# Optimization experiments

Hardware: AMD Instinct MI355X
Metric: run time of the kernel (lower is better)

Reference implementation:

```python
import jax, jax.numpy as jnp
import numpy as np


def setup_inputs() -> dict:
    key = jax.random.key(0)
    k_x, k_W, k_b, k_ids, k_w = jax.random.split(key, 5)
    N_ADAPTERS, D_OUT, D_IN = 32, 1024, 1024
    B, S = 2, 2048
    K = 8  # number of active adapters
    x = jax.random.normal(k_x, (B, S, D_IN), dtype=jnp.float32)
    W = jax.random.normal(k_W, (N_ADAPTERS, D_OUT, D_IN), dtype=jnp.float32)
    b = jax.random.normal(k_b, (N_ADAPTERS, D_OUT), dtype=jnp.float32)
    ids = jax.random.randint(k_ids, (K,), 0, N_ADAPTERS, dtype=jnp.int64)
    weights = jax.random.uniform(k_w, (K,), dtype=jnp.float32)
    return {"x": x, "W": W, "b": b, "ids": ids, "weights": weights}


def reference(x, W, b, ids, weights):
    # Original: out_i = Linear_{ids[i]}(x); output = sum_i weights[i] * out_i
    Wsel = W[ids]  # [k, o, d]  gather of selected adapter weights
    bsel = b[ids]  # [k, o]
    # Fused weighted mixture of k small GEMMs (same math as loop + weighted sum)
    out = jnp.einsum("k,kod,bsd->bso", weights, Wsel, x)
    out = out + jnp.einsum("k,ko->o", weights, bsel)
    return out
```

## Files before the change

kernel.cpp:

```cpp
#include <hip/hip_runtime.h>
#include <hip/hip_bf16.h>
#include <stdint.h>


typedef __attribute__((ext_vector_type(8))) short short8;
typedef __attribute__((ext_vector_type(4))) float float4v;

#define DIMK 1024
#define DIMN 1024
#define DIMM 4096

__device__ __forceinline__ unsigned short f2bf_rtn(float f) {
  union { float f; unsigned u; } v; v.f = f;
  unsigned u = v.u;
  return (unsigned short)((u + 0x7fffu + ((u >> 16) & 1u)) >> 16);
}

__global__ __launch_bounds__(256) void prep_kernel(
    const float* __restrict__ x, const float* __restrict__ W,
    const float* __restrict__ bia, const int* __restrict__ ids,
    const float* __restrict__ wts,
    unsigned short* __restrict__ xb, unsigned short* __restrict__ Wc,
    float* __restrict__ bc, int K)
{
  const int bid = blockIdx.x;
  if (bid < 1024) {
    const int t  = bid * 256 + threadIdx.x;
    const int o  = t >> 8;
    const int d4 = (t & 255) << 2;
    float ax = 0.f, ay = 0.f, az = 0.f, aw = 0.f;
    for (int k = 0; k < K; ++k) {
      const float wk = wts[k];
      const float4 w4 = *reinterpret_cast<const float4*>(
          &W[((size_t)ids[k] << 20) + ((size_t)o << 10) + d4]);
      ax += wk * w4.x; ay += wk * w4.y; az += wk * w4.z; aw += wk * w4.w;
    }
    ushort4 r;
    r.x = f2bf_rtn(ax); r.y = f2bf_rtn(ay); r.z = f2bf_rtn(az); r.w = f2bf_rtn(aw);
    *reinterpret_cast<ushort4*>(&Wc[(size_t)t << 2]) = r;
    if (t < DIMN) {
      float s = 0.f;
      for (int k = 0; k < K; ++k) s += wts[k] * bia[ids[k] * DIMN + t];
      bc[t] = s;
    }
  } else {
    const size_t t = (size_t)(bid - 1024) * 256 + threadIdx.x;
    const float4 v = *reinterpret_cast<const float4*>(&x[t << 2]);
    ushort4 r;
    r.x = f2bf_rtn(v.x); r.y = f2bf_rtn(v.y); r.z = f2bf_rtn(v.z); r.w = f2bf_rtn(v.w);
    *reinterpret_cast<ushort4*>(&xb[t << 2]) = r;
  }
}

__device__ __forceinline__ void load_lds16(const void* g, void* l) {
  __builtin_amdgcn_global_load_lds(
      (const __attribute__((address_space(1))) void*)g,
      (__attribute__((address_space(3))) void*)l, 16, 0, 0);
}

__global__ __launch_bounds__(256) void gemm_kernel(
    const unsigned short* __restrict__ xb,
    const unsigned short* __restrict__ Wc,
    const float* __restrict__ bc,
    float* __restrict__ out)
{
  constexpr int BK = 32;
  __shared__ __align__(16) unsigned short As[128 * BK];
  __shared__ __align__(16) unsigned short Bs[128 * BK];

  const int tid  = threadIdx.x;
  const int wave = tid >> 6;
  const int lane = tid & 63;
  const int m0 = blockIdx.y * 128;
  const int n0 = blockIdx.x * 128;

  const int crow = lane >> 2;
  const int ccol = (lane & 3) << 3;
  const int cid0 = wave * 2;
  const unsigned short* gA0 = xb + (size_t)(m0 + cid0 * 16 + crow) * DIMK + ccol;
  const unsigned short* gA1 = gA0 + 16 * DIMK;
  const unsigned short* gB0 = Wc + (size_t)(n0 + cid0 * 16 + crow) * DIMK + ccol;
  const unsigned short* gB1 = gB0 + 16 * DIMK;
  unsigned short* lA0 = &As[cid0 * 512];
  unsigned short* lA1 = &As[cid0 * 512 + 512];
  unsigned short* lB0 = &Bs[cid0 * 512];
  unsigned short* lB1 = &Bs[cid0 * 512 + 512];

  const int wm0  = (wave >> 1) * 64;
  const int wn0  = (wave & 1) * 64;
  const int quad = lane >> 4;
  const int r16  = lane & 15;

  const float4v zero = {0.f, 0.f, 0.f, 0.f};
  float4v acc[4][4];
#pragma unroll
  for (int i = 0; i < 4; ++i)
#pragma unroll
    for (int j = 0; j < 4; ++j) acc[i][j] = zero;

  for (int k0 = 0; k0 < DIMK; k0 += BK) {
    load_lds16(gA0 + k0, lA0);
    load_lds16(gA1 + k0, lA1);
    load_lds16(gB0 + k0, lB0);
    load_lds16(gB1 + k0, lB1);
    __syncthreads();

    short8 af[4], bf[4];
#pragma unroll
    for (int mt = 0; mt < 4; ++mt)
      af[mt] = *reinterpret_cast<const short8*>(&As[(wm0 + mt * 16 + r16) * BK + quad * 8]);
#pragma unroll
    for (int nt = 0; nt < 4; ++nt)
      bf[nt] = *reinterpret_cast<const short8*>(&Bs[(wn0 + nt * 16 + r16) * BK + quad * 8]);

#pragma unroll
    for (int mt = 0; mt < 4; ++mt)
#pragma unroll
      for (int nt = 0; nt < 4; ++nt)
        acc[mt][nt] = __builtin_amdgcn_mfma_f32_16x16x32_bf16(af[mt], bf[nt], acc[mt][nt], 0, 0, 0);

    __syncthreads();
  }

#pragma unroll
  for (int nt = 0; nt < 4; ++nt) {
    const int col = n0 + wn0 + nt * 16 + r16;
    const float bias = bc[col];
#pragma unroll
    for (int mt = 0; mt < 4; ++mt) {
      const int rbase = m0 + wm0 + mt * 16 + quad * 4;
#pragma unroll
      for (int r = 0; r < 4; ++r)
        out[(size_t)(rbase + r) * DIMN + col] = acc[mt][nt][r] + bias;
    }
  }
}

extern "C" void kernel_launch(void* const* d_in, const int* in_sizes, int n_in,
                              void* d_out, int out_size, void* d_ws, size_t ws_size,
                              hipStream_t stream) {
  const float* x   = (const float*)d_in[0];
  const float* W   = (const float*)d_in[1];
  const float* b   = (const float*)d_in[2];
  const int*   ids = (const int*)d_in[3];
  const float* wts = (const float*)d_in[4];
  float* out = (float*)d_out;
  const int K = in_sizes[3];

  unsigned short* xb = (unsigned short*)d_ws;
  unsigned short* Wc = (unsigned short*)((char*)d_ws + (8u << 20));
  float*          bc = (float*)((char*)d_ws + (10u << 20));

  prep_kernel<<<5120, 256, 0, stream>>>(x, W, b, ids, wts, xb, Wc, bc, K);
  dim3 grid(DIMN / 128, DIMM / 128);
  gemm_kernel<<<grid, 256, 0, stream>>>(xb, Wc, bc, out);
}
```

Measured before the change: 209.3 us.

## Shrink GEMM M-tile to 64, double BK to 64, and XOR-swizzle LDS layout

```diff
diff --git a/kernel.cpp b/kernel.cpp
--- a/kernel.cpp
+++ b/kernel.cpp
@@ -58,43 +58,49 @@
       (__attribute__((address_space(3))) void*)l, 16, 0, 0);
 }
 
-__global__ __launch_bounds__(256) void gemm_kernel(
+__global__ __launch_bounds__(256, 2) void gemm_kernel(
     const unsigned short* __restrict__ xb,
     const unsigned short* __restrict__ Wc,
     const float* __restrict__ bc,
     float* __restrict__ out)
 {
-  constexpr int BK = 32;
-  __shared__ __align__(16) unsigned short As[128 * BK];
+  constexpr int BK = 64;
+  __shared__ __align__(16) unsigned short As[64 * BK];
   __shared__ __align__(16) unsigned short Bs[128 * BK];
 
   const int tid  = threadIdx.x;
   const int wave = tid >> 6;
   const int lane = tid & 63;
-  const int m0 = blockIdx.y * 128;
+  const int m0 = blockIdx.y * 64;
   const int n0 = blockIdx.x * 128;
 
-  const int crow = lane >> 2;
-  const int ccol = (lane & 3) << 3;
-  const int cid0 = wave * 2;
-  const unsigned short* gA0 = xb + (size_t)(m0 + cid0 * 16 + crow) * DIMK + ccol;
-  const unsigned short* gA1 = gA0 + 16 * DIMK;
-  const unsigned short* gB0 = Wc + (size_t)(n0 + cid0 * 16 + crow) * DIMK + ccol;
-  const unsigned short* gB1 = gB0 + 16 * DIMK;
-  unsigned short* lA0 = &As[cid0 * 512];
-  unsigned short* lA1 = &As[cid0 * 512 + 512];
-  unsigned short* lB0 = &Bs[cid0 * 512];
-  unsigned short* lB1 = &Bs[cid0 * 512 + 512];
+  const int srow = lane >> 3;
+  const int scol = (((lane & 7) ^ srow) << 3);
+  const unsigned short* gA0 = xb + (size_t)(m0 + wave * 16 + srow) * DIMK + scol;
+  const unsigned short* gA1 = gA0 + 8 * DIMK;
+  const unsigned short* gB0 = Wc + (size_t)(n0 + wave * 32 + srow) * DIMK + scol;
+  const unsigned short* gB1 = gB0 + 8 * DIMK;
+  const unsigned short* gB2 = gB0 + 16 * DIMK;
+  const unsigned short* gB3 = gB0 + 24 * DIMK;
+  unsigned short* lA0 = &As[wave * 16 * BK];
+  unsigned short* lA1 = lA0 + 8 * BK;
+  unsigned short* lB0 = &Bs[wave * 32 * BK];
+  unsigned short* lB1 = lB0 + 8 * BK;
+  unsigned short* lB2 = lB0 + 16 * BK;
+  unsigned short* lB3 = lB0 + 24 * BK;
 
-  const int wm0  = (wave >> 1) * 64;
-  const int wn0  = (wave & 1) * 64;
+  const int wm   = (wave >> 1) * 32;
+  const int wn   = (wave & 1) * 64;
   const int quad = lane >> 4;
   const int r16  = lane & 15;
+  const int rx   = r16 & 7;
+  const int po0  = ((quad ^ rx) << 3);
+  const int po1  = (((4 + quad) ^ rx) << 3);
 
   const float4v zero = {0.f, 0.f, 0.f, 0.f};
-  float4v acc[4][4];
+  float4v acc[2][4];
 #pragma unroll
-  for (int i = 0; i < 4; ++i)
+  for (int i = 0; i < 2; ++i)
 #pragma unroll
     for (int j = 0; j < 4; ++j) acc[i][j] = zero;
 
@@ -103,32 +109,36 @@
     load_lds16(gA1 + k0, lA1);
     load_lds16(gB0 + k0, lB0);
     load_lds16(gB1 + k0, lB1);
+    load_lds16(gB2 + k0, lB2);
+    load_lds16(gB3 + k0, lB3);
     __syncthreads();
 
-    short8 af[4], bf[4];
 #pragma unroll
-    for (int mt = 0; mt < 4; ++mt)
-      af[mt] = *reinterpret_cast<const short8*>(&As[(wm0 + mt * 16 + r16) * BK + quad * 8]);
+    for (int s = 0; s < 2; ++s) {
+      const int po = s ? po1 : po0;
+      short8 af[2], bf[4];
 #pragma unroll
-    for (int nt = 0; nt < 4; ++nt)
-      bf[nt] = *reinterpret_cast<const short8*>(&Bs[(wn0 + nt * 16 + r16) * BK + quad * 8]);
-
-#pragma unroll
-    for (int mt = 0; mt < 4; ++mt)
+      for (int mt = 0; mt < 2; ++mt)
+        af[mt] = *reinterpret_cast<const short8*>(&As[(wm + mt * 16 + r16) * BK + po]);
 #pragma unroll
       for (int nt = 0; nt < 4; ++nt)
-        acc[mt][nt] = __builtin_amdgcn_mfma_f32_16x16x32_bf16(af[mt], bf[nt], acc[mt][nt], 0, 0, 0);
-
+        bf[nt] = *reinterpret_cast<const short8*>(&Bs[(wn + nt * 16 + r16) * BK + po]);
+#pragma unroll
+      for (int mt = 0; mt < 2; ++mt)
+#pragma unroll
+        for (int nt = 0; nt < 4; ++nt)
+          acc[mt][nt] = __builtin_amdgcn_mfma_f32_16x16x32_bf16(af[mt], bf[nt], acc[mt][nt], 0, 0, 0);
+    }
     __syncthreads();
   }
 
 #pragma unroll
   for (int nt = 0; nt < 4; ++nt) {
-    const int col = n0 + wn0 + nt * 16 + r16;
+    const int col = n0 + wn + nt * 16 + r16;
     const float bias = bc[col];
 #pragma unroll
-    for (int mt = 0; mt < 4; ++mt) {
-      const int rbase = m0 + wm0 + mt * 16 + quad * 4;
+    for (int mt = 0; mt < 2; ++mt) {
+      const int rbase = m0 + wm + mt * 16 + quad * 4;
 #pragma unroll
       for (int r = 0; r < 4; ++r)
         out[(size_t)(rbase + r) * DIMN + col] = acc[mt][nt][r] + bias;
@@ -152,6 +162,6 @@
   float*          bc = (float*)((char*)d_ws + (10u << 20));
 
   prep_kernel<<<5120, 256, 0, stream>>>(x, W, b, ids, wts, xb, Wc, bc, K);
-  dim3 grid(DIMN / 128, DIMM / 128);
+  dim3 grid(DIMN / 128, DIMM / 64);
   gemm_kernel<<<grid, 256, 0, stream>>>(xb, Wc, bc, out);
 }
```

After: 201.9 us. 3.5% less time.
